# Performance work log

Measured on AMD Instinct MI355X. Metric: run time of the kernel, lower is better.

## Reference

```python
import jax, jax.numpy as jnp
import numpy as np

T, B, L = 1024, 128, 128


def setup_inputs() -> dict:
    key = jax.random.key(0)
    k1, k2, k3, k4, k5 = jax.random.split(key, 5)
    return {
        "predictions": jax.random.normal(k1, (T, B, L), dtype=jnp.float32),
        "targets": jax.random.randint(k2, (T, B), 0, L, dtype=jnp.int64),
        "mask": jnp.ones((T, B), dtype=jnp.int32),
        "transitions": jax.random.normal(k3, (L, L), dtype=jnp.float32),
        "start_scores": jax.random.normal(k4, (L,), dtype=jnp.float32),
        "end_scores": jax.random.normal(k5, (L,), dtype=jnp.float32),
    }


def _numerator(predictions, targets, maskf, transitions, start_scores, end_scores):
    batch_idx = jnp.arange(predictions.shape[1])
    # emission score of the gold tag at every step: [T, B]
    emit = jnp.take_along_axis(predictions, targets[:, :, None], axis=2)[..., 0]
    trans = transitions[targets[:-1], targets[1:]]  # [T-1, B]
    score = start_scores[targets[0]] + emit[0]
    score = score + jnp.sum((trans + emit[1:]) * maskf[1:], axis=0)
    last_idx = jnp.sum(maskf, axis=0).astype(jnp.int32) - 1
    score = score + end_scores[targets[last_idx, batch_idx]]
    return score  # [B]


def _denominator(predictions, maskb, transitions, start_scores, end_scores):
    score0 = start_scores + predictions[0]  # [B, L]

    def step(score, inp):
        pred_i, mask_i = inp  # [B, L], [B]
        # [B, L, L]: prev-label axis 1, next-label axis 2
        s = score[:, :, None] + transitions[None, :, :] + pred_i[:, None, :]
        new_score = jax.scipy.special.logsumexp(s, axis=1)
        score = jnp.where(mask_i[:, None], new_score, score)
        return score, None

    score, _ = jax.lax.scan(step, score0, (predictions[1:], maskb[1:]))
    score = score + end_scores
    return jax.scipy.special.logsumexp(score, axis=1)  # [B]


def reference(predictions, targets, mask, transitions, start_scores, end_scores):
    maskf = mask.astype(predictions.dtype)
    maskb = mask.astype(bool)
    num = _numerator(predictions, targets, maskf, transitions, start_scores, end_scores)
    den = _denominator(predictions, maskb, transitions, start_scores, end_scores)
    return jnp.mean(den - num)
```

## Files before the change

kernel.cpp:

```cpp
#include <hip/hip_runtime.h>
#include <math.h>

#define T_DIM 1024
#define B_DIM 128
#define L_DIM 128

__device__ __forceinline__ float readlane0_f32(float v) {
    return __uint_as_float(__builtin_amdgcn_readfirstlane(__float_as_uint(v)));
}

__global__ __launch_bounds__(512, 1)
void crf_den_kernel(const float* __restrict__ pred,
                    const int*   __restrict__ mask,
                    const float* __restrict__ trans,
                    const float* __restrict__ start_s,
                    const float* __restrict__ end_s,
                    float* __restrict__ den_out)
{
    const int b     = blockIdx.x;
    const int tid   = threadIdx.x;
    const int w     = tid >> 6;
    const int lane  = tid & 63;
    const int sub   = lane & 15;
    const int kq    = lane >> 4;
    const int state = w * 16 + sub;
    const int kbase = kq * 32;

    float etr[32];
#pragma unroll
    for (int ii = 0; ii < 32; ++ii)
        etr[ii] = __expf(trans[(kbase + ii) * L_DIM + state]);

    __shared__ __align__(16) float es_lds[2][4 * 132];
    __shared__ __align__(16) int   e_lds[2][8];
    __shared__ float fsum_lds[8];

    float u = __expf(start_s[state] + pred[b * L_DIM + state]);
    int   D = 0;

    float ep_next = __expf(pred[(1 * B_DIM + b) * L_DIM + state]);
    float p2      = pred[(2 * B_DIM + b) * L_DIM + state];
    int   mk_next = mask[1 * B_DIM + b];
    int   mk2     = mask[2 * B_DIM + b];

    for (int t = 1; t < T_DIM; ++t) {
        const float ep_cur = ep_next;
        const int   mk     = mk_next;
        const int tpre = (t + 2 < T_DIM) ? (t + 2) : (T_DIM - 1);
        const float p3  = pred[(tpre * B_DIM + b) * L_DIM + state];
        const int   mk3 = mask[tpre * B_DIM + b];
        ep_next = __expf(p2);
        p2 = p3; mk_next = mk2; mk2 = mk3;

        const int buf = t & 1;

        const unsigned ub      = __float_as_uint(readlane0_f32(u));
        const int      Ebiased = (int)(ub >> 23);
        const float    scale   = __uint_as_float((unsigned)(254 - Ebiased) << 23);
        const float    us      = u * scale;
        if (lane < 16) {
            float* dst = &es_lds[buf][state];
#pragma unroll
            for (int c = 0; c < 4; ++c) dst[c * 132] = us;
        }
        if (lane == 0) e_lds[buf][w] = Ebiased;

        asm volatile("s_waitcnt lgkmcnt(0)" ::: "memory");
        __builtin_amdgcn_s_barrier();
        __builtin_amdgcn_sched_barrier(0);

        const float* esb = &es_lds[buf][kq * 132 + kbase];
        const int4  eL = *(const int4*)&e_lds[buf][0];
        const int4  eH = *(const int4*)&e_lds[buf][4];

        float accA = 0.f, accB = 0.f;
#pragma unroll
        for (int c = 0; c < 4; ++c) {
            const float4 e4 = *(const float4*)&esb[c * 4];
            accA = fmaf(e4.x, etr[c * 4 + 0], accA);
            accA = fmaf(e4.y, etr[c * 4 + 1], accA);
            accA = fmaf(e4.z, etr[c * 4 + 2], accA);
            accA = fmaf(e4.w, etr[c * 4 + 3], accA);
        }
#pragma unroll
        for (int c = 4; c < 8; ++c) {
            const float4 e4 = *(const float4*)&esb[c * 4];
            accB = fmaf(e4.x, etr[c * 4 + 0], accB);
            accB = fmaf(e4.y, etr[c * 4 + 1], accB);
            accB = fmaf(e4.z, etr[c * 4 + 2], accB);
            accB = fmaf(e4.w, etr[c * 4 + 3], accB);
        }

        const int emax = max(max(max(eL.x, eL.y), max(eL.z, eL.w)),
                             max(max(eH.x, eH.y), max(eH.z, eH.w)));
        int eA, eB;
        switch (kq) {
            case 0: eA = eL.x; eB = eL.y; break;
            case 1: eA = eL.z; eB = eL.w; break;
            case 2: eA = eH.x; eB = eH.y; break;
            default: eA = eH.z; eB = eH.w; break;
        }
        float part = ldexpf(accA, eA - emax) + ldexpf(accB, eB - emax);
        part += __shfl_xor(part, 16, 64);
        part += __shfl_xor(part, 32, 64);

        if (mk) { u = part * ep_cur; D += (emax - 127); }
    }

    float val = (kq == 0) ? u * __expf(end_s[state]) : 0.f;
#pragma unroll
    for (int off = 32; off >= 1; off >>= 1)
        val += __shfl_xor(val, off, 64);
    if (lane == 0) fsum_lds[w] = val;
    __syncthreads();
    if (tid == 0) {
        float tot = 0.f;
#pragma unroll
        for (int ww = 0; ww < 8; ++ww) tot += fsum_lds[ww];
        den_out[b] = logf(tot) + (float)D * 0.69314718055994531f;
    }
}

__global__ __launch_bounds__(256, 1)
void crf_num_kernel(const float* __restrict__ pred,
                    const int*   __restrict__ targets,
                    const int*   __restrict__ mask,
                    const float* __restrict__ trans,
                    const float* __restrict__ start_s,
                    const float* __restrict__ end_s,
                    float* __restrict__ num_out)
{
    const int b = blockIdx.x;
    const int k = threadIdx.x;

    float local = 0.f;
    int   msum  = 0;
    for (int t = k; t < T_DIM; t += 256) {
        const int mk = mask[t * B_DIM + b];
        msum += mk;
        if (t >= 1) {
            const int tp = targets[(t - 1) * B_DIM + b];
            const int tc = targets[t * B_DIM + b];
            const float c = trans[tp * L_DIM + tc] +
                            pred[(t * B_DIM + b) * L_DIM + tc];
            local += c * (float)mk;
        }
    }

#pragma unroll
    for (int off = 32; off >= 1; off >>= 1) {
        local += __shfl_xor(local, off, 64);
        msum  += __shfl_xor(msum,  off, 64);
    }
    __shared__ float sred[4];
    __shared__ int   ired[4];
    const int w = k >> 6;
    if ((k & 63) == 0) { sred[w] = local; ired[w] = msum; }
    __syncthreads();
    if (k == 0) {
        float tot = sred[0] + sred[1] + sred[2] + sred[3];
        const int ms = ired[0] + ired[1] + ired[2] + ired[3];
        const int t0 = targets[b];
        tot += start_s[t0] + pred[b * L_DIM + t0];
        const int last = ms - 1;
        tot += end_s[targets[last * B_DIM + b]];
        num_out[b] = tot;
    }
}

__global__ __launch_bounds__(128, 1)
void crf_reduce_kernel(const float* __restrict__ den,
                       const float* __restrict__ num,
                       float* __restrict__ out)
{
    const int j = threadIdx.x;
    float d = den[j] - num[j];
#pragma unroll
    for (int off = 32; off >= 1; off >>= 1)
        d += __shfl_xor(d, off, 64);
    __shared__ float s[2];
    if ((j & 63) == 0) s[j >> 6] = d;
    __syncthreads();
    if (j == 0) out[0] = (s[0] + s[1]) * (1.0f / (float)B_DIM);
}

extern "C" void kernel_launch(void* const* d_in, const int* in_sizes, int n_in,
                              void* d_out, int out_size, void* d_ws, size_t ws_size,
                              hipStream_t stream)
{
    const float* pred    = (const float*)d_in[0];
    const int*   targets = (const int*)  d_in[1];
    const int*   mask    = (const int*)  d_in[2];
    const float* trans   = (const float*)d_in[3];
    const float* start_s = (const float*)d_in[4];
    const float* end_s   = (const float*)d_in[5];
    float* out = (float*)d_out;

    float* den = (float*)d_ws;
    float* num = den + B_DIM;

    crf_den_kernel<<<B_DIM, 512, 0, stream>>>(pred, mask, trans, start_s, end_s, den);
    crf_num_kernel<<<B_DIM, 256, 0, stream>>>(pred, targets, mask, trans, start_s, end_s, num);
    crf_reduce_kernel<<<1, 128, 0, stream>>>(den, num, out);
}
```

Before: 735.7 us.

## Recast CRF forward recursion as bf16 MFMA matmuls with pre-exponentiated emissions

Replaces the per-sequence scalar FMA recursion (128 blocks of 512 threads, an LDS barrier every step) with an MFMA path: 4 single-wave blocks each carry 32 sequences. Each step is a 128x128 by 128x32 bf16 matmul held entirely in registers, with permlane swaps turning the output into the next B operand. A prep kernel pre-exponentiates and re-lays out the emissions into workspace so the loop streams them with vector loads. Renormalisation runs only every fourth step, and a fallback keeps the old path when the workspace is too small. This risks bf16 precision loss, serial MFMA latency on only 4 waves, and extra memory traffic to write and read the exp buffer.

Result: slower. 1.341 ms (+82.3%).

```diff
diff --git a/kernel.cpp b/kernel.cpp
--- a/kernel.cpp
+++ b/kernel.cpp
@@ -5,8 +5,211 @@
 #define B_DIM 128
 #define L_DIM 128
 
+using bf16x8 = __attribute__((ext_vector_type(8))) __bf16;
+using f32x16 = __attribute__((ext_vector_type(16))) float;
+using v4i    = __attribute__((ext_vector_type(4))) int;
+using f4     = __attribute__((ext_vector_type(4))) float;
+
+__device__ __forceinline__ int cvtpk_bf16(float lo, float hi) {
+    int r;
+    asm("v_cvt_pk_bf16_f32 %0, %1, %2" : "=v"(r) : "v"(lo), "v"(hi));
+    return r;
+}
+
+__device__ __forceinline__ void plswap(int &a, int &b) {
+    auto r = __builtin_amdgcn_permlane32_swap(a, b, false, false);
+    a = r[0];
+    b = r[1];
+}
+
 __device__ __forceinline__ float readlane0_f32(float v) {
     return __uint_as_float(__builtin_amdgcn_readfirstlane(__float_as_uint(v)));
+}
+
+__global__ __launch_bounds__(256)
+void crf_prep(const float* __restrict__ pred, const int* __restrict__ mask,
+              float* __restrict__ ep, int* __restrict__ mkp)
+{
+    const int gid = blockIdx.x * 256 + threadIdx.x;
+#pragma unroll
+    for (int s = 0; s < 2; ++s) {
+        const int idx4 = gid * 2 + s;
+        const int k4 = idx4 & 15;
+        const int l  = (idx4 >> 4) & 63;
+        const int g  = (idx4 >> 10) & 3;
+        const int t  = idx4 >> 12;
+        const int c  = l & 31, hh = l >> 5;
+        const int bb = g * 32 + c;
+        const int rt = k4 >> 2, q = k4 & 3;
+        const int rowbase = 32 * rt + 8 * q + 4 * hh;
+        const f4 p = *(const f4*)&pred[((size_t)t * B_DIM + bb) * L_DIM + rowbase];
+        f4 e;
+        e[0] = __expf(p[0]); e[1] = __expf(p[1]);
+        e[2] = __expf(p[2]); e[3] = __expf(p[3]);
+        *(f4*)&ep[(size_t)idx4 * 4] = e;
+    }
+    if (gid < 1026 * B_DIM) {
+        const int t = gid >> 7;
+        const int cc = gid & 127;
+        mkp[gid] = mask[(t < T_DIM ? t : T_DIM - 1) * B_DIM + cc];
+    }
+}
+
+template <int RN>
+__device__ __forceinline__ void den_step(
+    const bf16x8 (&Afr)[4][8], v4i (&Bw)[8], const f32x16 &Zf,
+    f4 (&EX)[16], int &MKX, const f4*& EPP, const int*& MPP, int &Dc)
+{
+    const bool mkb = (MKX != 0);
+
+    f32x16 dd[4];
+#pragma unroll
+    for (int rt = 0; rt < 4; ++rt) {
+        f32x16 a = __builtin_amdgcn_mfma_f32_32x32x16_bf16(
+            Afr[rt][0], __builtin_bit_cast(bf16x8, Bw[0]), Zf, 0, 0, 0);
+#pragma unroll
+        for (int ks = 1; ks < 8; ++ks)
+            a = __builtin_amdgcn_mfma_f32_32x32x16_bf16(
+                Afr[rt][ks], __builtin_bit_cast(bf16x8, Bw[ks]), a, 0, 0, 0);
+        dd[rt] = a;
+    }
+
+#pragma unroll
+    for (int rt = 0; rt < 4; ++rt)
+#pragma unroll
+        for (int reg = 0; reg < 16; ++reg)
+            dd[rt][reg] *= EX[rt * 4 + (reg >> 2)][reg & 3];
+
+#pragma unroll
+    for (int i = 0; i < 16; ++i) EX[i] = EPP[i];
+    EPP += 8192;
+    const int mknew = *MPP; MPP += 2 * B_DIM;
+
+    if (RN) {
+        float mx = 0.f;
+#pragma unroll
+        for (int rt = 0; rt < 4; ++rt)
+#pragma unroll
+            for (int reg = 0; reg < 16; ++reg)
+                mx = fmaxf(mx, __builtin_fabsf(dd[rt][reg]));
+        mx = fmaxf(mx, __shfl_xor(mx, 32, 64));
+        const int eb = (int)((__float_as_uint(mx) >> 23) & 255);
+        const float sc = __uint_as_float((unsigned)(254 - eb) << 23);
+#pragma unroll
+        for (int rt = 0; rt < 4; ++rt)
+#pragma unroll
+            for (int reg = 0; reg < 16; ++reg)
+                dd[rt][reg] *= sc;
+        if (mkb) Dc += eb - 127;
+    }
+
+#pragma unroll
+    for (int rt = 0; rt < 4; ++rt) {
+        int w0 = cvtpk_bf16(dd[rt][0],  dd[rt][1]);
+        int w1 = cvtpk_bf16(dd[rt][2],  dd[rt][3]);
+        int w2 = cvtpk_bf16(dd[rt][4],  dd[rt][5]);
+        int w3 = cvtpk_bf16(dd[rt][6],  dd[rt][7]);
+        int w4 = cvtpk_bf16(dd[rt][8],  dd[rt][9]);
+        int w5 = cvtpk_bf16(dd[rt][10], dd[rt][11]);
+        int w6 = cvtpk_bf16(dd[rt][12], dd[rt][13]);
+        int w7 = cvtpk_bf16(dd[rt][14], dd[rt][15]);
+        plswap(w0, w2); plswap(w1, w3);
+        plswap(w4, w6); plswap(w5, w7);
+        Bw[2*rt][0]   = mkb ? w0 : Bw[2*rt][0];
+        Bw[2*rt][1]   = mkb ? w1 : Bw[2*rt][1];
+        Bw[2*rt][2]   = mkb ? w2 : Bw[2*rt][2];
+        Bw[2*rt][3]   = mkb ? w3 : Bw[2*rt][3];
+        Bw[2*rt+1][0] = mkb ? w4 : Bw[2*rt+1][0];
+        Bw[2*rt+1][1] = mkb ? w5 : Bw[2*rt+1][1];
+        Bw[2*rt+1][2] = mkb ? w6 : Bw[2*rt+1][2];
+        Bw[2*rt+1][3] = mkb ? w7 : Bw[2*rt+1][3];
+    }
+    MKX = mknew;
+}
+
+__global__ __launch_bounds__(64, 1)
+void crf_den_mfma(const float* __restrict__ pred,
+                  const float* __restrict__ trans,
+                  const float* __restrict__ start_s,
+                  const float* __restrict__ end_s,
+                  const float* __restrict__ ep,
+                  const int*   __restrict__ mkp,
+                  float* __restrict__ den_out)
+{
+    const int g    = blockIdx.x;
+    const int lane = threadIdx.x;
+    const int c    = lane & 31;
+    const int hi   = lane >> 5;
+    const int b    = g * 32 + c;
+
+    bf16x8 Afr[4][8];
+#pragma unroll
+    for (int rt = 0; rt < 4; ++rt)
+#pragma unroll
+        for (int ks = 0; ks < 8; ++ks)
+#pragma unroll
+            for (int r = 0; r < 8; ++r) {
+                const int kg = 16 * ks + 8 * hi + r;
+                const int m  = 32 * rt + c;
+                Afr[rt][ks][r] = (__bf16)__expf(trans[kg * L_DIM + m]);
+            }
+
+    v4i Bw[8];
+#pragma unroll
+    for (int ks = 0; ks < 8; ++ks)
+#pragma unroll
+        for (int w = 0; w < 4; ++w) {
+            const int k0 = 16 * ks + 8 * hi + 2 * w;
+            const float u0 = __expf(start_s[k0]     + pred[(size_t)b * L_DIM + k0]);
+            const float u1 = __expf(start_s[k0 + 1] + pred[(size_t)b * L_DIM + k0 + 1]);
+            Bw[ks][w] = cvtpk_bf16(u0, u1);
+        }
+
+    f32x16 Zf;
+#pragma unroll
+    for (int k = 0; k < 16; ++k) Zf[k] = 0.0f;
+
+    const f4* epA = (const f4*)(ep + (size_t)1 * 16384 + g * 4096 + lane * 64);
+    const f4* epB = (const f4*)(ep + (size_t)2 * 16384 + g * 4096 + lane * 64);
+    f4 EA[16], EB[16];
+#pragma unroll
+    for (int i = 0; i < 16; ++i) EA[i] = epA[i];
+    epA += 8192;
+#pragma unroll
+    for (int i = 0; i < 16; ++i) EB[i] = epB[i];
+    epB += 8192;
+    const int* mpA = mkp + 1 * B_DIM + b;
+    const int* mpB = mkp + 2 * B_DIM + b;
+    int mkA = *mpA; mpA += 2 * B_DIM;
+    int mkB = *mpB; mpB += 2 * B_DIM;
+    int Dc = 0;
+
+#pragma unroll 1
+    for (int it = 0; it < 255; ++it) {
+        den_step<0>(Afr, Bw, Zf, EA, mkA, epA, mpA, Dc);
+        den_step<0>(Afr, Bw, Zf, EB, mkB, epB, mpB, Dc);
+        den_step<0>(Afr, Bw, Zf, EA, mkA, epA, mpA, Dc);
+        den_step<1>(Afr, Bw, Zf, EB, mkB, epB, mpB, Dc);
+    }
+    den_step<0>(Afr, Bw, Zf, EA, mkA, epA, mpA, Dc);
+    den_step<0>(Afr, Bw, Zf, EB, mkB, epB, mpB, Dc);
+    den_step<0>(Afr, Bw, Zf, EA, mkA, epA, mpA, Dc);
+
+    float csum = 0.f;
+#pragma unroll
+    for (int ks = 0; ks < 8; ++ks)
+#pragma unroll
+        for (int w = 0; w < 4; ++w) {
+            const int dw = Bw[ks][w];
+            const int k0 = 16 * ks + 8 * hi + 2 * w;
+            const float lo = __uint_as_float(((unsigned)dw & 0xffffu) << 16);
+            const float hh = __uint_as_float((unsigned)dw & 0xffff0000u);
+            csum += lo * __expf(end_s[k0]);
+            csum += hh * __expf(end_s[k0 + 1]);
+        }
+    csum += __shfl_xor(csum, 32, 64);
+    if (hi == 0)
+        den_out[b] = logf(csum) + (float)Dc * 0.69314718055994531f;
 }
 
 __global__ __launch_bounds__(512, 1)
@@ -53,7 +256,6 @@
         p2 = p3; mk_next = mk2; mk2 = mk3;
 
         const int buf = t & 1;
-
         const unsigned ub      = __float_as_uint(readlane0_f32(u));
         const int      Ebiased = (int)(ub >> 23);
         const float    scale   = __uint_as_float((unsigned)(254 - Ebiased) << 23);
@@ -61,7 +263,7 @@
         if (lane < 16) {
             float* dst = &es_lds[buf][state];
 #pragma unroll
-            for (int c = 0; c < 4; ++c) dst[c * 132] = us;
+            for (int cc = 0; cc < 4; ++cc) dst[cc * 132] = us;
         }
         if (lane == 0) e_lds[buf][w] = Ebiased;
 
@@ -70,35 +272,35 @@
         __builtin_amdgcn_sched_barrier(0);
 
         const float* esb = &es_lds[buf][kq * 132 + kbase];
-        const int4  eL = *(const int4*)&e_lds[buf][0];
-        const int4  eH = *(const int4*)&e_lds[buf][4];
+        const v4i  eL = *(const v4i*)&e_lds[buf][0];
+        const v4i  eH = *(const v4i*)&e_lds[buf][4];
 
         float accA = 0.f, accB = 0.f;
 #pragma unroll
-        for (int c = 0; c < 4; ++c) {
-            const float4 e4 = *(const float4*)&esb[c * 4];
-            accA = fmaf(e4.x, etr[c * 4 + 0], accA);
-            accA = fmaf(e4.y, etr[c * 4 + 1], accA);
-            accA = fmaf(e4.z, etr[c * 4 + 2], accA);
-            accA = fmaf(e4.w, etr[c * 4 + 3], accA);
-        }
-#pragma unroll
-        for (int c = 4; c < 8; ++c) {
-            const float4 e4 = *(const float4*)&esb[c * 4];
-            accB = fmaf(e4.x, etr[c * 4 + 0], accB);
-            accB = fmaf(e4.y, etr[c * 4 + 1], accB);
-            accB = fmaf(e4.z, etr[c * 4 + 2], accB);
-            accB = fmaf(e4.w, etr[c * 4 + 3], accB);
-        }
-
-        const int emax = max(max(max(eL.x, eL.y), max(eL.z, eL.w)),
-                             max(max(eH.x, eH.y), max(eH.z, eH.w)));
+        for (int cc = 0; cc < 4; ++cc) {
+            const f4 e4 = *(const f4*)&esb[cc * 4];
+            accA = fmaf(e4[0], etr[cc*4+0], accA);
+            accA = fmaf(e4[1], etr[cc*4+1], accA);
+            accA = fmaf(e4[2], etr[cc*4+2], accA);
+            accA = fmaf(e4[3], etr[cc*4+3], accA);
+        }
+#pragma unroll
+        for (int cc = 4; cc < 8; ++cc) {
+            const f4 e4 = *(const f4*)&esb[cc * 4];
+            accB = fmaf(e4[0], etr[cc*4+0], accB);
+            accB = fmaf(e4[1], etr[cc*4+1], accB);
+            accB = fmaf(e4[2], etr[cc*4+2], accB);
+            accB = fmaf(e4[3], etr[cc*4+3], accB);
+        }
+
+        const int emax = max(max(max(eL[0], eL[1]), max(eL[2], eL[3])),
+                             max(max(eH[0], eH[1]), max(eH[2], eH[3])));
         int eA, eB;
         switch (kq) {
-            case 0: eA = eL.x; eB = eL.y; break;
-            case 1: eA = eL.z; eB = eL.w; break;
-            case 2: eA = eH.x; eB = eH.y; break;
-            default: eA = eH.z; eB = eH.w; break;
+            case 0: eA = eL[0]; eB = eL[1]; break;
+            case 1: eA = eL[2]; eB = eL[3]; break;
+            case 2: eA = eH[0]; eB = eH[1]; break;
+            default: eA = eH[2]; eB = eH[3]; break;
         }
         float part = ldexpf(accA, eA - emax) + ldexpf(accB, eB - emax);
         part += __shfl_xor(part, 16, 64);
@@ -141,9 +343,9 @@
         if (t >= 1) {
             const int tp = targets[(t - 1) * B_DIM + b];
             const int tc = targets[t * B_DIM + b];
-            const float c = trans[tp * L_DIM + tc] +
-                            pred[(t * B_DIM + b) * L_DIM + tc];
-            local += c * (float)mk;
+            const float cc = trans[tp * L_DIM + tc] +
+                             pred[((size_t)t * B_DIM + b) * L_DIM + tc];
+            local += cc * (float)mk;
         }
     }
 
@@ -161,7 +363,7 @@
         float tot = sred[0] + sred[1] + sred[2] + sred[3];
         const int ms = ired[0] + ired[1] + ired[2] + ired[3];
         const int t0 = targets[b];
-        tot += start_s[t0] + pred[b * L_DIM + t0];
+        tot += start_s[t0] + pred[(size_t)b * L_DIM + t0];
         const int last = ms - 1;
         tot += end_s[targets[last * B_DIM + b]];
         num_out[b] = tot;
@@ -196,10 +398,28 @@
     const float* end_s   = (const float*)d_in[5];
     float* out = (float*)d_out;
 
-    float* den = (float*)d_ws;
-    float* num = den + B_DIM;
-
-    crf_den_kernel<<<B_DIM, 512, 0, stream>>>(pred, mask, trans, start_s, end_s, den);
-    crf_num_kernel<<<B_DIM, 256, 0, stream>>>(pred, targets, mask, trans, start_s, end_s, num);
-    crf_reduce_kernel<<<1, 128, 0, stream>>>(den, num, out);
-}
+    const size_t EPF  = (size_t)1026 * 16384;
+    const size_t MPI  = (size_t)1026 * 128;
+    const size_t NEED = (EPF + MPI + 256) * sizeof(float);
+
+    if (ws_size >= NEED) {
+        float* ep  = (float*)d_ws;
+        int*   mkp = (int*)(ep + EPF);
+        float* den = (float*)(mkp + MPI);
+        float* num = den + B_DIM;
+        crf_prep<<<8192, 256, 0, stream>>>(pred, mask, ep, mkp);
+        crf_num_kernel<<<B_DIM, 256, 0, stream>>>(pred, targets, mask, trans,
+                                                  start_s, end_s, num);
+        crf_den_mfma<<<4, 64, 0, stream>>>(pred, trans, start_s, end_s,
+                                           ep, mkp, den);
+        crf_reduce_kernel<<<1, 128, 0, stream>>>(den, num, out);
+    } else {
+        float* den = (float*)d_ws;
+        float* num = den + B_DIM;
+        crf_den_kernel<<<B_DIM, 512, 0, stream>>>(pred, mask, trans,
+                                                  start_s, end_s, den);
+        crf_num_kernel<<<B_DIM, 256, 0, stream>>>(pred, targets, mask, trans,
+                                                  start_s, end_s, num);
+        crf_reduce_kernel<<<1, 128, 0, stream>>>(den, num, out);
+    }
+}
```
